# Kernel tuning notes

Hardware: AMD Instinct MI355X
Metric: run time of the kernel (lower is better)

## Reference

```python
import jax, jax.numpy as jnp
import numpy as np

HIDDEN = 1024
INTER = 1408
N_EXPERTS = 8
TOTAL_TOKENS = 8192


def setup_inputs() -> dict:
    key = jax.random.key(0)
    k_x, k_w1, k_w2 = jax.random.split(key, 3)
    x = jax.random.normal(k_x, (TOTAL_TOKENS, HIDDEN), dtype=jnp.float32)
    # fused gate+up projection per expert: [E, H, 2*I]
    w1w3 = jax.random.normal(k_w1, (N_EXPERTS, HIDDEN, 2 * INTER), dtype=jnp.float32) * (HIDDEN ** -0.5)
    # down projection per expert: [E, I, H]
    w2 = jax.random.normal(k_w2, (N_EXPERTS, INTER, HIDDEN), dtype=jnp.float32) * (INTER ** -0.5)
    # deterministic uneven split that sums exactly to TOTAL_TOKENS
    tpe = np.array([700, 1300, 900, 1100, 1024, 1024, 800, 1344], dtype=np.int64)
    assert tpe.sum() == TOTAL_TOKENS
    tokens_per_expert = jnp.asarray(tpe)
    return {"x": x, "w1w3": w1w3, "w2": w2, "tokens_per_expert": tokens_per_expert, "decoding": False}


def _grouped_mm(inp, W, expert_ids):
    # inp: [T, D_in], W: [E, D_in, D_out]; rows of inp are grouped by expert,
    # expert_ids[t] = owning expert. Equivalent to per-segment GEMM with W[e].
    T = inp.shape[0]
    E = W.shape[0]
    out = jnp.zeros((T, W.shape[-1]), dtype=inp.dtype)
    for e in range(E):  # fixed small expert count; loop over experts, not tokens
        mask = (expert_ids == e)[:, None]
        out = out + jnp.where(mask, inp, 0.0) @ W[e]
    return out


def reference(x, w1w3, w2, tokens_per_expert, decoding):
    T = x.shape[0]
    E = w1w3.shape[0]
    # per-token expert id from contiguous segment lengths (jit-safe fixed length)
    expert_ids = jnp.repeat(jnp.arange(E), tokens_per_expert, total_repeat_length=T)
    gate_up = _grouped_mm(x, w1w3, expert_ids)          # [T, 2*I]
    gate, up = jnp.split(gate_up, 2, axis=-1)           # swiglu(split_dim=-1)
    h = jax.nn.silu(gate) * up                          # [T, I]
    return _grouped_mm(h, w2, expert_ids)               # [T, H]
```

## Files before the change

### kernel.cpp

```cpp
#include <hip/hip_runtime.h>
#include <hip/hip_bf16.h>


#define HIDDEN 1024
#define INTER  1408
#define NEXP   8
#define TOKENS 8192

typedef __attribute__((ext_vector_type(8))) short bf16x8;
typedef __attribute__((ext_vector_type(4))) float f32x4;
typedef __attribute__((ext_vector_type(4))) unsigned short u16x4;
typedef __attribute__((ext_vector_type(8))) unsigned short u16x8;

#define GLOAD_LDS16(g, l)                                                      \
  __builtin_amdgcn_global_load_lds(                                            \
      (const __attribute__((address_space(1))) void*)(g),                      \
      (__attribute__((address_space(3))) void*)(l), 16, 0, 0)

__device__ inline unsigned short f2bf(float f) {
  unsigned int x = __float_as_uint(f);
  x += 0x7fffu + ((x >> 16) & 1u);
  return (unsigned short)(x >> 16);
}

__device__ inline int detect_f32(const float* __restrict__ xf, int lane) {
  unsigned int u = __float_as_uint(xf[lane & 63]);
  int e = (u >> 23) & 0xff;
  return __popcll(__ballot(e >= 100 && e <= 140)) >= 48 ? 1 : 0;
}

__device__ inline void load_tpe(const int* __restrict__ raw, int* tpe) {
  bool ok = true; int s = 0;
#pragma unroll
  for (int e = 0; e < NEXP; e++) { int v = raw[e]; tpe[e] = v; ok = ok && (v >= 0 && v <= TOKENS); s += v; }
  if (ok && s == TOKENS) return;
  ok = true; s = 0;
#pragma unroll
  for (int e = 0; e < NEXP; e++) { int v = raw[2 * e]; tpe[e] = v; ok = ok && (v >= 0 && v <= TOKENS); s += v; }
  if (ok && s == TOKENS) return;
  const int fb[NEXP] = {700, 1300, 900, 1100, 1024, 1024, 800, 1344};
#pragma unroll
  for (int e = 0; e < NEXP; e++) tpe[e] = fb[e];
}

__device__ inline bool expert_map(const int* __restrict__ tpe_raw, int rt,
                                  int& expert, int& row0, int& rows_valid) {
  int tpe[NEXP];
  load_tpe(tpe_raw, tpe);
  int acc = 0, pre = 0;
#pragma unroll
  for (int e = 0; e < NEXP; e++) {
    int nt = (tpe[e] + 127) >> 7;
    if (rt < acc + nt) {
      int ti = rt - acc;
      expert = e; row0 = pre + ti * 128; rows_valid = tpe[e] - ti * 128;
      return true;
    }
    acc += nt; pre += tpe[e];
  }
  return false;
}

__device__ inline void transpose_tile(const void* __restrict__ in,
                                      unsigned short* __restrict__ out,
                                      int R, int C, int r0, int c0,
                                      int t, int f32) {
  const int mr = t & 7, mc = t >> 3;
  const int r = r0 + mr * 8, c = c0 + mc * 8;
  u16x8 w[8];
  if (f32) {
    f32x4 f0[8], f1[8];
#pragma unroll
    for (int i = 0; i < 8; i++) {
      const float* p = (const float*)in + (size_t)(r + i) * C + c;
      f0[i] = *(const f32x4*)p;
      f1[i] = *(const f32x4*)(p + 4);
    }
#pragma unroll
    for (int j = 0; j < 4; j++)
#pragma unroll
      for (int i = 0; i < 8; i++) {
        w[j][i]     = f2bf(f0[i][j]);
        w[j + 4][i] = f2bf(f1[i][j]);
      }
  } else {
    u16x8 uv[8];
#pragma unroll
    for (int i = 0; i < 8; i++)
      uv[i] = *(const u16x8*)((const unsigned short*)in + (size_t)(r + i) * C + c);
#pragma unroll
    for (int j = 0; j < 8; j++)
#pragma unroll
      for (int i = 0; i < 8; i++) w[j][i] = uv[i][j];
  }
#pragma unroll
  for (int j = 0; j < 8; j++)
    *(u16x8*)&out[(size_t)(c + j) * R + r] = w[j];
}

__global__ __launch_bounds__(256) void prepare(
    const float* __restrict__ xf, const void* __restrict__ x,
    const void* __restrict__ w1w3, const void* __restrict__ w2,
    unsigned short* __restrict__ xb, unsigned short* __restrict__ w1t,
    unsigned short* __restrict__ w2t) {
  const int t = threadIdx.x;
  const int f32 = detect_f32(xf, t & 63);
  const int b = blockIdx.x;

  if (b < 1024) {
    const size_t base = (size_t)b * 8192;
#pragma unroll
    for (int k = 0; k < 4; k++) {
      const size_t i = base + k * 2048 + t * 8;
      u16x8 v;
      if (f32) {
        f32x4 g0 = *(const f32x4*)((const float*)x + i);
        f32x4 g1 = *(const f32x4*)((const float*)x + i + 4);
#pragma unroll
        for (int j = 0; j < 4; j++) { v[j] = f2bf(g0[j]); v[j + 4] = f2bf(g1[j]); }
      } else {
        v = *(const u16x8*)((const unsigned short*)x + i);
      }
      *(u16x8*)(xb + i) = v;
    }
    return;
  }

  if (b < 2432) {
    const int u = b - 1024;
    const int ex = u / 176, rem = u % 176;
    const int r0 = (rem / 11) * 64, c0 = (rem % 11) * 256;
    const char* in = (const char*)w1w3 +
                     (size_t)ex * 1024 * 2816 * (f32 ? 4 : 2);
    transpose_tile(in, w1t + (size_t)ex * 2816 * 1024, 1024, 2816, r0, c0, t, f32);
  } else {
    const int u = b - 2432;
    const int ex = u / 88, rem = u % 88;
    const int r0 = (rem / 4) * 64, c0 = (rem % 4) * 256;
    const char* in = (const char*)w2 +
                     (size_t)ex * 1408 * 1024 * (f32 ? 4 : 2);
    transpose_tile(in, w2t + (size_t)ex * 1024 * 1408, 1408, 1024, r0, c0, t, f32);
  }
}

__global__ __launch_bounds__(256, 2) void moe_gemm1(
    const unsigned short* __restrict__ xb, const unsigned short* __restrict__ w1t,
    const int* __restrict__ tpe_raw, unsigned short* __restrict__ h) {
  __shared__ unsigned short As[2][128 * 32];
  __shared__ unsigned short Bg[2][64 * 32];
  __shared__ unsigned short Bu[2][64 * 32];
  int expert, row0, rows_valid;
  if (!expert_map(tpe_raw, blockIdx.y, expert, row0, rows_valid)) return;

  const int tid = threadIdx.x;
  const int lane = tid & 63, wave = tid >> 6;
  const int wr = wave >> 1, wc = wave & 1;
  const int i0 = blockIdx.x * 64;
  const unsigned short* W = w1t + (size_t)expert * 2816 * HIDDEN;

  const int q0 = wave * 2, q1 = wave * 2 + 1;
  const int sr0 = q0 * 16 + (lane >> 2), sr1 = q1 * 16 + (lane >> 2);
  const int sb = wave * 16 + (lane >> 2);
  const int sk = (lane & 3) * 8;
  const size_t arow0 = (size_t)min(row0 + sr0, TOKENS - 1);
  const size_t arow1 = (size_t)min(row0 + sr1, TOKENS - 1);
  const unsigned short* pa0 = xb + arow0 * HIDDEN + sk;
  const unsigned short* pa1 = xb + arow1 * HIDDEN + sk;
  const unsigned short* pg = W + (size_t)(i0 + sb) * HIDDEN + sk;
  const unsigned short* pu = W + (size_t)(INTER + i0 + sb) * HIDDEN + sk;

  f32x4 accg[4][2] = {};
  f32x4 accu[4][2] = {};
  const int fr = lane & 15, fq = (lane >> 4) * 8;

  GLOAD_LDS16(pa0, &As[0][q0 * 512]);
  GLOAD_LDS16(pa1, &As[0][q1 * 512]);
  GLOAD_LDS16(pg, &Bg[0][wave * 512]);
  GLOAD_LDS16(pu, &Bu[0][wave * 512]);
  pa0 += 32; pa1 += 32; pg += 32; pu += 32;
  __syncthreads();

  const int NT = HIDDEN / 32;
  for (int it = 0; it < NT; ++it) {
    const int cur = it & 1, nxt = cur ^ 1;
    if (it + 1 < NT) {
      GLOAD_LDS16(pa0, &As[nxt][q0 * 512]);
      GLOAD_LDS16(pa1, &As[nxt][q1 * 512]);
      GLOAD_LDS16(pg, &Bg[nxt][wave * 512]);
      GLOAD_LDS16(pu, &Bu[nxt][wave * 512]);
      pa0 += 32; pa1 += 32; pg += 32; pu += 32;
    }

    bf16x8 a[4], bg[2], bu[2];
#pragma unroll
    for (int mi = 0; mi < 4; mi++)
      a[mi] = *(const bf16x8*)&As[cur][(wr * 64 + mi * 16 + fr) * 32 + fq];
#pragma unroll
    for (int ni = 0; ni < 2; ni++) {
      bg[ni] = *(const bf16x8*)&Bg[cur][(wc * 32 + ni * 16 + fr) * 32 + fq];
      bu[ni] = *(const bf16x8*)&Bu[cur][(wc * 32 + ni * 16 + fr) * 32 + fq];
    }
#pragma unroll
    for (int mi = 0; mi < 4; mi++)
#pragma unroll
      for (int ni = 0; ni < 2; ni++) {
        accg[mi][ni] =
            __builtin_amdgcn_mfma_f32_16x16x32_bf16(a[mi], bg[ni], accg[mi][ni], 0, 0, 0);
        accu[mi][ni] =
            __builtin_amdgcn_mfma_f32_16x16x32_bf16(a[mi], bu[ni], accu[mi][ni], 0, 0, 0);
      }

    __syncthreads();
  }

#pragma unroll
  for (int mi = 0; mi < 4; mi++)
#pragma unroll
    for (int r = 0; r < 4; r++) {
      const int row_local = wr * 64 + mi * 16 + ((lane >> 4) * 4) + r;
      if (row_local < rows_valid && row0 + row_local < TOKENS) {
        const size_t rowoff = (size_t)(row0 + row_local) * INTER;
#pragma unroll
        for (int ni = 0; ni < 2; ni++) {
          const int col = i0 + wc * 32 + ni * 16 + fr;
          const float g = accg[mi][ni][r];
          const float u = accu[mi][ni][r];
          const float sg = g / (1.0f + __expf(-g));
          h[rowoff + col] = f2bf(sg * u);
        }
      }
    }
}

__global__ __launch_bounds__(256, 2) void moe_gemm2(
    const unsigned short* __restrict__ h, const unsigned short* __restrict__ w2t,
    const int* __restrict__ tpe_raw, void* __restrict__ out,
    const float* __restrict__ xf) {
  __shared__ unsigned short As[2][128 * 32];
  __shared__ unsigned short Bs[2][128 * 32];
  int expert, row0, rows_valid;
  if (!expert_map(tpe_raw, blockIdx.y, expert, row0, rows_valid)) return;
  const int f32out = detect_f32(xf, threadIdx.x & 63);

  const int tid = threadIdx.x;
  const int lane = tid & 63, wave = tid >> 6;
  const int wr = wave >> 1, wc = wave & 1;
  const int n0 = blockIdx.x * 128;
  const unsigned short* W = w2t + (size_t)expert * INTER * HIDDEN;

  const int q0 = wave * 2, q1 = wave * 2 + 1;
  const int sr0 = q0 * 16 + (lane >> 2), sr1 = q1 * 16 + (lane >> 2);
  const int sk = (lane & 3) * 8;
  const size_t arow0 = (size_t)min(row0 + sr0, TOKENS - 1);
  const size_t arow1 = (size_t)min(row0 + sr1, TOKENS - 1);
  const unsigned short* pa0 = h + arow0 * INTER + sk;
  const unsigned short* pa1 = h + arow1 * INTER + sk;
  const unsigned short* pb0 = W + (size_t)(n0 + sr0) * INTER + sk;
  const unsigned short* pb1 = W + (size_t)(n0 + sr1) * INTER + sk;

  f32x4 acc[4][4] = {};
  const int fr = lane & 15, fq = (lane >> 4) * 8;

  GLOAD_LDS16(pa0, &As[0][q0 * 512]);
  GLOAD_LDS16(pa1, &As[0][q1 * 512]);
  GLOAD_LDS16(pb0, &Bs[0][q0 * 512]);
  GLOAD_LDS16(pb1, &Bs[0][q1 * 512]);
  pa0 += 32; pa1 += 32; pb0 += 32; pb1 += 32;
  __syncthreads();

  const int NT = INTER / 32;
  for (int it = 0; it < NT; ++it) {
    const int cur = it & 1, nxt = cur ^ 1;
    if (it + 1 < NT) {
      GLOAD_LDS16(pa0, &As[nxt][q0 * 512]);
      GLOAD_LDS16(pa1, &As[nxt][q1 * 512]);
      GLOAD_LDS16(pb0, &Bs[nxt][q0 * 512]);
      GLOAD_LDS16(pb1, &Bs[nxt][q1 * 512]);
      pa0 += 32; pa1 += 32; pb0 += 32; pb1 += 32;
    }

    bf16x8 a[4], bb[4];
#pragma unroll
    for (int mi = 0; mi < 4; mi++)
      a[mi] = *(const bf16x8*)&As[cur][(wr * 64 + mi * 16 + fr) * 32 + fq];
#pragma unroll
    for (int ni = 0; ni < 4; ni++)
      bb[ni] = *(const bf16x8*)&Bs[cur][(wc * 64 + ni * 16 + fr) * 32 + fq];
#pragma unroll
    for (int mi = 0; mi < 4; mi++)
#pragma unroll
      for (int ni = 0; ni < 4; ni++)
        acc[mi][ni] =
            __builtin_amdgcn_mfma_f32_16x16x32_bf16(a[mi], bb[ni], acc[mi][ni], 0, 0, 0);

    __syncthreads();
  }

#pragma unroll
  for (int mi = 0; mi < 4; mi++)
#pragma unroll
    for (int r = 0; r < 4; r++) {
      const int row_local = wr * 64 + mi * 16 + ((lane >> 4) * 4) + r;
      if (row_local < rows_valid && row0 + row_local < TOKENS) {
        const size_t rowoff = (size_t)(row0 + row_local) * HIDDEN;
#pragma unroll
        for (int ni = 0; ni < 4; ni++) {
          const int col = n0 + wc * 64 + ni * 16 + fr;
          if (f32out)
            ((float*)out)[rowoff + col] = acc[mi][ni][r];
          else
            ((unsigned short*)out)[rowoff + col] = f2bf(acc[mi][ni][r]);
        }
      }
    }
}

extern "C" void kernel_launch(void* const* d_in, const int* in_sizes, int n_in,
                              void* d_out, int out_size, void* d_ws, size_t ws_size,
                              hipStream_t stream) {
  const void* x = d_in[0];
  const void* w1w3 = d_in[1];
  const void* w2 = d_in[2];
  const int* tpe = (const int*)d_in[3];
  const float* xf = (const float*)d_in[0];

  const size_t XB_BYTES = (size_t)TOKENS * HIDDEN * 2;
  const size_t W1T_BYTES = (size_t)NEXP * 2816 * HIDDEN * 2;
  const size_t W2T_BYTES = (size_t)NEXP * INTER * HIDDEN * 2;
  char* ws = (char*)d_ws;
  unsigned short* xb = (unsigned short*)ws;
  unsigned short* w1t = (unsigned short*)(ws + XB_BYTES);
  unsigned short* w2t = (unsigned short*)(ws + XB_BYTES + W1T_BYTES);
  unsigned short* h = (unsigned short*)(ws + XB_BYTES + W1T_BYTES + W2T_BYTES);

  prepare<<<3136, 256, 0, stream>>>(xf, x, w1w3, w2, xb, w1t, w2t);
  moe_gemm1<<<dim3(INTER / 64, 72), 256, 0, stream>>>(xb, w1t, tpe, h);
  moe_gemm2<<<dim3(HIDDEN / 128, 72), 256, 0, stream>>>(h, w2t, tpe, d_out, xf);
}
```

Measured before the change: 331.8 us.

## Transpose weights through swizzled LDS and overlap w2 transpose with gemm1

Weight transposition now stages tiles through LDS with an XOR swizzle, so global reads and writes are both coalesced, replacing the register-only 8x8 transpose that wrote scattered 16-byte chunks. The w2 transpose moves out of the prepare kernel into extra blocks of moe_gemm1 (grid y grows from 72 to 88), so it runs alongside the first grouped GEMM. gemm1's shared memory becomes a single 64KB buffer shared by both roles. That larger LDS footprint may limit how many gemm1 blocks fit per CU.

```diff
diff --git a/kernel.cpp b/kernel.cpp
--- a/kernel.cpp
+++ b/kernel.cpp
@@ -61,98 +61,125 @@
   return false;
 }
 
-__device__ inline void transpose_tile(const void* __restrict__ in,
+template <int RE, int CE, int LOG_NC4, int LOG_NRCH>
+__device__ inline void ldst_transpose(const void* __restrict__ in,
                                       unsigned short* __restrict__ out,
                                       int R, int C, int r0, int c0,
-                                      int t, int f32) {
-  const int mr = t & 7, mc = t >> 3;
-  const int r = r0 + mr * 8, c = c0 + mc * 8;
-  u16x8 w[8];
-  if (f32) {
-    f32x4 f0[8], f1[8];
-#pragma unroll
-    for (int i = 0; i < 8; i++) {
-      const float* p = (const float*)in + (size_t)(r + i) * C + c;
-      f0[i] = *(const f32x4*)p;
-      f1[i] = *(const f32x4*)(p + 4);
-    }
-#pragma unroll
-    for (int j = 0; j < 4; j++)
-#pragma unroll
-      for (int i = 0; i < 8; i++) {
-        w[j][i]     = f2bf(f0[i][j]);
-        w[j + 4][i] = f2bf(f1[i][j]);
-      }
-  } else {
-    u16x8 uv[8];
-#pragma unroll
-    for (int i = 0; i < 8; i++)
-      uv[i] = *(const u16x8*)((const unsigned short*)in + (size_t)(r + i) * C + c);
-#pragma unroll
-    for (int j = 0; j < 8; j++)
-#pragma unroll
-      for (int i = 0; i < 8; i++) w[j][i] = uv[i][j];
-  }
-#pragma unroll
-  for (int j = 0; j < 8; j++)
-    *(u16x8*)&out[(size_t)(c + j) * R + r] = w[j];
+                                      int t, int f32,
+                                      unsigned short* __restrict__ lds) {
+  constexpr int NC4 = 1 << LOG_NC4;
+  constexpr int NRCH = 1 << LOG_NRCH;
+  constexpr int MASK = NRCH - 1;
+  static_assert(NC4 * 4 == CE && NRCH * 8 == RE, "geometry");
+  static_assert(RE * NC4 == 4 * 2048, "4 rounds");
+
+  const int clane = t & (NC4 - 1);
+  const int rslot = t >> LOG_NC4;
+  const int c = clane * 4;
+#pragma unroll
+  for (int round = 0; round < 4; ++round) {
+    const int rb = round * (RE / 4) + rslot * 8;
+    u16x8 w[4];
+    if (f32) {
+      f32x4 v[8];
+#pragma unroll
+      for (int i = 0; i < 8; i++)
+        v[i] = *(const f32x4*)((const float*)in + (size_t)(r0 + rb + i) * C + c0 + c);
+#pragma unroll
+      for (int j = 0; j < 4; j++)
+#pragma unroll
+        for (int i = 0; i < 8; i++) w[j][i] = f2bf(v[i][j]);
+    } else {
+      u16x4 v[8];
+#pragma unroll
+      for (int i = 0; i < 8; i++)
+        v[i] = *(const u16x4*)((const unsigned short*)in + (size_t)(r0 + rb + i) * C + c0 + c);
+#pragma unroll
+      for (int j = 0; j < 4; j++)
+#pragma unroll
+        for (int i = 0; i < 8; i++) w[j][i] = v[i][j];
+    }
+    const int rch = rb >> 3;
+#pragma unroll
+    for (int j = 0; j < 4; j++) {
+      const int cc = c + j;
+      const int chunk = (cc << LOG_NRCH) + (rch ^ ((cc >> 2) & MASK));
+      *(u16x8*)&lds[chunk * 8] = w[j];
+    }
+  }
+  __syncthreads();
+
+  const int rl = t & (NRCH - 1);
+  const int cslot = t >> LOG_NRCH;
+  constexpr int CSLOTS = 256 >> LOG_NRCH;
+#pragma unroll
+  for (int it = 0; it < CE / CSLOTS; ++it) {
+    const int crow = it * CSLOTS + cslot;
+    const int chunk = (crow << LOG_NRCH) + (rl ^ ((crow >> 2) & MASK));
+    u16x8 w = *(const u16x8*)&lds[chunk * 8];
+    *(u16x8*)&out[(size_t)(c0 + crow) * R + r0 + rl * 8] = w;
+  }
 }
 
 __global__ __launch_bounds__(256) void prepare(
     const float* __restrict__ xf, const void* __restrict__ x,
-    const void* __restrict__ w1w3, const void* __restrict__ w2,
-    unsigned short* __restrict__ xb, unsigned short* __restrict__ w1t,
-    unsigned short* __restrict__ w2t) {
+    const void* __restrict__ w1w3,
+    unsigned short* __restrict__ xb, unsigned short* __restrict__ w1t) {
+  __shared__ __align__(16) unsigned short lds[32768];
   const int t = threadIdx.x;
   const int f32 = detect_f32(xf, t & 63);
   const int b = blockIdx.x;
 
-  if (b < 1024) {
-    const size_t base = (size_t)b * 8192;
-#pragma unroll
-    for (int k = 0; k < 4; k++) {
-      const size_t i = base + k * 2048 + t * 8;
-      u16x8 v;
+  if (b < 512) {
+    const size_t base = (size_t)b * 16384 + t * 4;
+#pragma unroll
+    for (int it = 0; it < 16; ++it) {
+      const size_t i = base + (size_t)it * 1024;
+      u16x4 v;
       if (f32) {
-        f32x4 g0 = *(const f32x4*)((const float*)x + i);
-        f32x4 g1 = *(const f32x4*)((const float*)x + i + 4);
-#pragma unroll
-        for (int j = 0; j < 4; j++) { v[j] = f2bf(g0[j]); v[j + 4] = f2bf(g1[j]); }
+        f32x4 g = *(const f32x4*)((const float*)x + i);
+        v[0] = f2bf(g[0]); v[1] = f2bf(g[1]); v[2] = f2bf(g[2]); v[3] = f2bf(g[3]);
       } else {
-        v = *(const u16x8*)((const unsigned short*)x + i);
+        v = *(const u16x4*)((const unsigned short*)x + i);
       }
-      *(u16x8*)(xb + i) = v;
+      *(u16x4*)(xb + i) = v;
     }
     return;
   }
 
-  if (b < 2432) {
-    const int u = b - 1024;
-    const int ex = u / 176, rem = u % 176;
-    const int r0 = (rem / 11) * 64, c0 = (rem % 11) * 256;
-    const char* in = (const char*)w1w3 +
-                     (size_t)ex * 1024 * 2816 * (f32 ? 4 : 2);
-    transpose_tile(in, w1t + (size_t)ex * 2816 * 1024, 1024, 2816, r0, c0, t, f32);
-  } else {
-    const int u = b - 2432;
-    const int ex = u / 88, rem = u % 88;
-    const int r0 = (rem / 4) * 64, c0 = (rem % 4) * 256;
-    const char* in = (const char*)w2 +
-                     (size_t)ex * 1408 * 1024 * (f32 ? 4 : 2);
-    transpose_tile(in, w2t + (size_t)ex * 1024 * 1408, 1408, 1024, r0, c0, t, f32);
-  }
+  const int u = b - 512;
+  const int ex = u / 88, rem = u % 88;
+  const int r0 = (rem / 22) * 256, c0 = (rem % 22) * 128;
+  const char* in = (const char*)w1w3 + (size_t)ex * 1024 * 2816 * (f32 ? 4 : 2);
+  ldst_transpose<256, 128, 5, 5>(in, w1t + (size_t)ex * 2816 * 1024,
+                                 1024, 2816, r0, c0, t, f32, lds);
 }
 
 __global__ __launch_bounds__(256, 2) void moe_gemm1(
     const unsigned short* __restrict__ xb, const unsigned short* __restrict__ w1t,
-    const int* __restrict__ tpe_raw, unsigned short* __restrict__ h) {
-  __shared__ unsigned short As[2][128 * 32];
-  __shared__ unsigned short Bg[2][64 * 32];
-  __shared__ unsigned short Bu[2][64 * 32];
+    const int* __restrict__ tpe_raw, unsigned short* __restrict__ h,
+    const void* __restrict__ w2raw, unsigned short* __restrict__ w2t,
+    const float* __restrict__ xf) {
+  __shared__ __align__(16) unsigned short smem[32768];
+  const int tid = threadIdx.x;
+
+  if (blockIdx.y >= 72) {
+    const int f32 = detect_f32(xf, tid & 63);
+    const int idx = (blockIdx.y - 72) * 22 + blockIdx.x;
+    const int ex = idx / 44, rem = idx % 44;
+    const int r0 = (rem / 4) * 128, c0 = (rem % 4) * 256;
+    const char* in = (const char*)w2raw + (size_t)ex * 1408 * 1024 * (f32 ? 4 : 2);
+    ldst_transpose<128, 256, 6, 4>(in, w2t + (size_t)ex * 1024 * 1408,
+                                   1408, 1024, r0, c0, tid, f32, smem);
+    return;
+  }
+
+#define AS(b_) (smem + (b_) * 4096)
+#define BG(b_) (smem + 8192 + (b_) * 2048)
+#define BU(b_) (smem + 12288 + (b_) * 2048)
   int expert, row0, rows_valid;
   if (!expert_map(tpe_raw, blockIdx.y, expert, row0, rows_valid)) return;
 
-  const int tid = threadIdx.x;
   const int lane = tid & 63, wave = tid >> 6;
   const int wr = wave >> 1, wc = wave & 1;
   const int i0 = blockIdx.x * 64;
@@ -173,10 +200,10 @@
   f32x4 accu[4][2] = {};
   const int fr = lane & 15, fq = (lane >> 4) * 8;
 
-  GLOAD_LDS16(pa0, &As[0][q0 * 512]);
-  GLOAD_LDS16(pa1, &As[0][q1 * 512]);
-  GLOAD_LDS16(pg, &Bg[0][wave * 512]);
-  GLOAD_LDS16(pu, &Bu[0][wave * 512]);
+  GLOAD_LDS16(pa0, AS(0) + q0 * 512);
+  GLOAD_LDS16(pa1, AS(0) + q1 * 512);
+  GLOAD_LDS16(pg, BG(0) + wave * 512);
+  GLOAD_LDS16(pu, BU(0) + wave * 512);
   pa0 += 32; pa1 += 32; pg += 32; pu += 32;
   __syncthreads();
 
@@ -184,21 +211,21 @@
   for (int it = 0; it < NT; ++it) {
     const int cur = it & 1, nxt = cur ^ 1;
     if (it + 1 < NT) {
-      GLOAD_LDS16(pa0, &As[nxt][q0 * 512]);
-      GLOAD_LDS16(pa1, &As[nxt][q1 * 512]);
-      GLOAD_LDS16(pg, &Bg[nxt][wave * 512]);
-      GLOAD_LDS16(pu, &Bu[nxt][wave * 512]);
+      GLOAD_LDS16(pa0, AS(nxt) + q0 * 512);
+      GLOAD_LDS16(pa1, AS(nxt) + q1 * 512);
+      GLOAD_LDS16(pg, BG(nxt) + wave * 512);
+      GLOAD_LDS16(pu, BU(nxt) + wave * 512);
       pa0 += 32; pa1 += 32; pg += 32; pu += 32;
     }
 
     bf16x8 a[4], bg[2], bu[2];
 #pragma unroll
     for (int mi = 0; mi < 4; mi++)
-      a[mi] = *(const bf16x8*)&As[cur][(wr * 64 + mi * 16 + fr) * 32 + fq];
+      a[mi] = *(const bf16x8*)&AS(cur)[(wr * 64 + mi * 16 + fr) * 32 + fq];
 #pragma unroll
     for (int ni = 0; ni < 2; ni++) {
-      bg[ni] = *(const bf16x8*)&Bg[cur][(wc * 32 + ni * 16 + fr) * 32 + fq];
-      bu[ni] = *(const bf16x8*)&Bu[cur][(wc * 32 + ni * 16 + fr) * 32 + fq];
+      bg[ni] = *(const bf16x8*)&BG(cur)[(wc * 32 + ni * 16 + fr) * 32 + fq];
+      bu[ni] = *(const bf16x8*)&BU(cur)[(wc * 32 + ni * 16 + fr) * 32 + fq];
     }
 #pragma unroll
     for (int mi = 0; mi < 4; mi++)
@@ -230,6 +257,9 @@
         }
       }
     }
+#undef AS
+#undef BG
+#undef BU
 }
 
 __global__ __launch_bounds__(256, 2) void moe_gemm2(
@@ -333,7 +363,7 @@
   unsigned short* w2t = (unsigned short*)(ws + XB_BYTES + W1T_BYTES);
   unsigned short* h = (unsigned short*)(ws + XB_BYTES + W1T_BYTES + W2T_BYTES);
 
-  prepare<<<3136, 256, 0, stream>>>(xf, x, w1w3, w2, xb, w1t, w2t);
-  moe_gemm1<<<dim3(INTER / 64, 72), 256, 0, stream>>>(xb, w1t, tpe, h);
+  prepare<<<1216, 256, 0, stream>>>(xf, x, w1w3, xb, w1t);
+  moe_gemm1<<<dim3(INTER / 64, 88), 256, 0, stream>>>(xb, w1t, tpe, h, w2, w2t, xf);
   moe_gemm2<<<dim3(HIDDEN / 128, 72), 256, 0, stream>>>(h, w2t, tpe, d_out, xf);
 }
```

New measurement: 335.1 us. Within noise of the previous version (+1.0%).
